# Optimization experiments

Hardware: AMD Instinct MI355X
Metric: run time of the kernel (lower is better)

## Reference

```python
import jax, jax.numpy as jnp
import numpy as np

B, S, E, HID, NTR, NCAL, CW, VOCAB, POS = 4096, 201, 32, 512, 4, 8, 16, 32, 256
LN_EPS = 1e-5


def _ln(x, g, b):
    m = x.mean(-1, keepdims=True)
    v = ((x - m) ** 2).mean(-1, keepdims=True)
    return (x - m) * jax.lax.rsqrt(v + LN_EPS) * g + b


def setup_inputs() -> dict:
    key = jax.random.key(0)
    ks = jax.random.split(key, 24)
    g = lambda i, shape, s=0.1: (jax.random.normal(ks[i], shape, jnp.float32) * s)
    return dict(
        encoded_seq=jax.random.randint(ks[0], (B, S), 0, VOCAB, jnp.int32),
        experiment_id=jax.random.randint(ks[1], (B,), 0, NCAL, jnp.int32),
        tok_emb=g(2, (VOCAB, E), 1.0),
        pos_emb=g(3, (POS, E), 1.0),
        ln1_g=jnp.ones((NTR, E)), ln1_b=jnp.zeros((NTR, E)),
        wq=g(4, (NTR, E, E)), wk=g(5, (NTR, E, E)), wv=g(6, (NTR, E, E)),
        bq=g(7, (NTR, E), 0.01), bk=g(8, (NTR, E), 0.01), bv=g(9, (NTR, E), 0.01),
        wo=g(10, (NTR, E, E)), bo=g(11, (NTR, E), 0.01),
        ln2_g=jnp.ones((NTR, E)), ln2_b=jnp.zeros((NTR, E)),
        w1=g(12, (NTR, E, HID)), b1=g(13, (NTR, HID), 0.01),
        w2=g(14, (NTR, HID, E)), b2=g(15, (NTR, E), 0.01),
        lnf_g=jnp.ones((E,)), lnf_b=jnp.zeros((E,)),
        wpen=g(16, (E, 1)), bpen=g(17, (1,), 0.01),
        wfan=g(18, (1, CW)), bfan=g(19, (CW,), 0.01),
        wcal=g(20, (NCAL, CW, 1)), bcal=g(21, (NCAL, 1), 0.01),
    )


def reference(encoded_seq, experiment_id, tok_emb, pos_emb,
              ln1_g, ln1_b, wq, wk, wv, bq, bk, bv, wo, bo,
              ln2_g, ln2_b, w1, b1, w2, b2,
              lnf_g, lnf_b, wpen, bpen, wfan, bfan, wcal, bcal):
    # embedding + positional add: [B,S,E]
    x = tok_emb[encoded_seq] + pos_emb[jnp.arange(S)]
    scale = 1.0 / jnp.sqrt(jnp.float32(E))  # num_heads=1 => head_dim=E
    for i in range(NTR):
        n = _ln(x, ln1_g[i], ln1_b[i])
        q = n @ wq[i] + bq[i]
        k = n @ wk[i] + bk[i]
        v = n @ wv[i] + bv[i]
        a = jax.nn.softmax(jnp.einsum('bqe,bke->bqk', q, k) * scale, axis=-1)
        att = jnp.einsum('bqk,bke->bqe', a, v) @ wo[i] + bo[i]
        x = x + att
        h = _ln(x, ln2_g[i], ln2_b[i])
        x = x + (jax.nn.silu(h @ w1[i] + b1[i]) @ w2[i] + b2[i])
    contrib = _ln(x, lnf_g, lnf_b) @ wpen + bpen        # [B,S,1]
    underlying = contrib.sum(axis=-2)                    # [B,1]
    pre = jax.nn.elu(underlying @ wfan + bfan)           # [B,CW]
    # all calibrator heads at once: [B,NCAL]
    all_corr = jnp.einsum('bc,ncj->bn', pre, wcal) + bcal[:, 0]
    mask = jax.nn.one_hot(experiment_id, NCAL, dtype=pre.dtype)  # exactly the (exp==id) mask-sum
    corrected = (all_corr * mask).sum(-1, keepdims=True) + underlying
    return corrected.squeeze()
```

## Files before the change

### kernel.cpp

```cpp
#include <hip/hip_runtime.h>


#define SS   201
#define SP   208
#define NMT  13
#define EE   32
#define HIDN 512
#define NTRL 4
#define CWN  16
#define BB   4096
#define XST  36
#define K2ST 20
#define VWST 108

#define X_OFF    0
#define K2_OFF   14976
#define VW2_OFF  31616
#define SMEM_SZ  45440

#define WS_FRAG  0
#define WS_BIAS  294912
#define WS_B1    299008
#define WS_FIN   307200
#define L2E      1.4426950408889634f
#define QCE      0.2550546813f

typedef unsigned short u16;
typedef unsigned int   u32;
typedef short bf16x4 __attribute__((ext_vector_type(4)));
typedef short bf16x8 __attribute__((ext_vector_type(8)));
typedef float f32x4  __attribute__((ext_vector_type(4)));
typedef float f32x2  __attribute__((ext_vector_type(2)));

__device__ __forceinline__ f32x4 MF(bf16x8 a, bf16x8 b, f32x4 c){
  return __builtin_amdgcn_mfma_f32_16x16x32_bf16(a, b, c, 0, 0, 0);
}
__device__ __forceinline__ float bf2f(u16 u){ return __uint_as_float(((u32)u)<<16); }
__device__ __forceinline__ u16 f2bf(float f){
  u32 u = __float_as_uint(f);
  u += 0x7fffu + ((u>>16)&1u);
  return (u16)(u>>16);
}
__device__ __forceinline__ u32 pk2bf(f32x2 v){
#if defined(__has_builtin) && __has_builtin(__builtin_amdgcn_cvt_pk_bf16_f32)
  auto r = __builtin_amdgcn_cvt_pk_bf16_f32(v.x, v.y);
  u32 u; __builtin_memcpy(&u, &r, 4); return u;
#else
  return ((__float_as_uint(v.x)+0x8000u)>>16) | ((__float_as_uint(v.y)+0x8000u) & 0xffff0000u);
#endif
}
__device__ __forceinline__ f32x2 upk2(u32 d){
  return f32x2{ __uint_as_float(d<<16), __uint_as_float(d & 0xffff0000u) };
}
template<bool F32>
__device__ __forceinline__ float ldv(const void* p, int i){
  if (F32) return ((const float*)p)[i];
  return bf2f(((const u16*)p)[i]);
}
template<bool F32>
__device__ __forceinline__ u16 ldbf(const void* p, int i){
  if (F32) return f2bf(((const float*)p)[i]);
  return ((const u16*)p)[i];
}
__device__ __forceinline__ bf16x8 mk8(u32 a0, u32 a1, u32 a2, u32 a3){
  u32 t[4] = {a0,a1,a2,a3};
  bf16x8 r; __builtin_memcpy(&r, t, 16); return r;
}
__device__ __forceinline__ bf16x8 dup8(bf16x4 v){
  bf16x8 r = {v[0],v[0],v[1],v[1],v[2],v[2],v[3],v[3]};
  return r;
}
__device__ __forceinline__ u32 spk(f32x2 z){
  const f32x2 nl2e2 = {-L2E, -L2E};
  const f32x2 one2  = {1.f, 1.f};
  f32x2 a = z * nl2e2;
  f32x2 e = { __builtin_amdgcn_exp2f(a.x), __builtin_amdgcn_exp2f(a.y) };
  f32x2 d = one2 + e;
  f32x2 rc = { __builtin_amdgcn_rcpf(d.x), __builtin_amdgcn_rcpf(d.y) };
  f32x2 s = z * rc;
  return pk2bf(s);
}

__device__ __forceinline__ int sniff_bf16(const void* tok_emb, int tid){
  int sane = 0;
  if (tid < 64){
    u16 wd = ((const u16*)tok_emb)[tid];
    int e = (wd >> 7) & 0xFF;
    sane = (e >= 100 && e <= 140) ? 1 : 0;
  }
  return (__syncthreads_count(sane) >= 52) ? 1 : 0;
}

template<bool F32>
__device__ __forceinline__ void frag_body(const void* wq, const void* wk,
    const void* wv, const void* wo, const void* w1, const void* w2, void* ws)
{
  int t = blockIdx.x;
  int l = t / 72, k = t % 72;
  int lane = threadIdx.x, l16 = lane & 15, quad = lane >> 4;
  bf16x8 v;
  if (k < 8){
    int mat = k >> 1, half = k & 1;
    if (mat == 2){
      int col = half*16 + l16;
      #pragma unroll
      for (int j=0;j<8;j++){
        int a = quad*8 + j;
        float acc = 0.f;
        for (int e=0;e<EE;e++)
          acc += ldv<F32>(wv, l*1024 + a*32 + e) * ldv<F32>(wo, l*1024 + e*32 + col);
        v[j] = (short)f2bf(acc);
      }
    } else if (mat == 0){
      #pragma unroll
      for (int j=0;j<8;j++)
        v[j] = (short)f2bf(QCE * ldv<F32>(wq, l*1024 + (quad*8+j)*32 + half*16 + l16));
    } else {
      const void* src = (mat==1)? wk : wo;
      #pragma unroll
      for (int j=0;j<8;j++)
        v[j] = (short)ldbf<F32>(src, l*1024 + (quad*8+j)*32 + half*16 + l16);
    }
  } else if (k < 40){
    int nt = k - 8;
    #pragma unroll
    for (int j=0;j<8;j++)
      v[j] = (short)ldbf<F32>(w1, l*16384 + (quad*8+j)*512 + nt*16 + l16);
  } else {
    int kc = (k-40)>>1, nh = (k-40)&1;
    #pragma unroll
    for (int j=0;j<8;j++){
      int hh = kc*32 + ((j&4) ? 16 : 0) + quad*4 + (j&3);
      v[j] = (short)ldbf<F32>(w2, l*16384 + hh*32 + nh*16 + l16);
    }
  }
  *(bf16x8*)((char*)ws + WS_FRAG + t*1024 + lane*16) = v;
}

__global__ __launch_bounds__(64) void fmt_frags(
    const void* __restrict__ tok_emb,
    const void* __restrict__ wq, const void* __restrict__ wk,
    const void* __restrict__ wv, const void* __restrict__ wo,
    const void* __restrict__ w1, const void* __restrict__ w2,
    void* __restrict__ ws)
{
  if (sniff_bf16(tok_emb, threadIdx.x)) frag_body<false>(wq,wk,wv,wo,w1,w2,ws);
  else                                  frag_body<true >(wq,wk,wv,wo,w1,w2,ws);
}

template<bool F32>
__device__ __forceinline__ void bias_body(
    const void* bq, const void* bk, const void* bv, const void* wo, const void* bo,
    const void* ln1_g, const void* ln1_b, const void* ln2_g, const void* ln2_b,
    const void* b1, const void* b2,
    const void* lnf_g, const void* lnf_b, const void* wpen, const void* bpen,
    const void* wfan, const void* bfan, const void* wcal, const void* bcal,
    void* ws)
{
  int tid = threadIdx.x, idx = tid & 31, grp = tid >> 5;
  float* BW  = (float*)((char*)ws + WS_BIAS);
  float* BW1 = (float*)((char*)ws + WS_B1);
  float* FW  = (float*)((char*)ws + WS_FIN);
  for (int l=0;l<NTRL;l++){
    float v = 0.f;
    switch(grp){
      case 0: v = QCE * ldv<F32>(bq, l*32+idx); break;
      case 1: v = ldv<F32>(bk, l*32+idx); break;
      case 2: {
        float acc = ldv<F32>(bo, l*32+idx);
        for (int e=0;e<EE;e++) acc += ldv<F32>(bv, l*32+e) * ldv<F32>(wo, l*1024 + e*32 + idx);
        v = acc; break;
      }
      case 3: v = ldv<F32>(ln1_g, l*32+idx); break;
      case 4: v = ldv<F32>(ln1_b, l*32+idx); break;
      case 5: v = ldv<F32>(ln2_g, l*32+idx); break;
      case 6: v = ldv<F32>(ln2_b, l*32+idx); break;
      case 7: v = ldv<F32>(b2,   l*32+idx); break;
    }
    BW[l*256 + tid] = v;
  }
  for (int i=tid; i<NTRL*HIDN; i+=256) BW1[i] = ldv<F32>(b1, i);
  if (tid < 32){
    FW[tid]    = ldv<F32>(lnf_g, tid);
    FW[32+tid] = ldv<F32>(lnf_b, tid);
    FW[64+tid] = ldv<F32>(wpen, tid);
  }
  if (tid == 0) FW[96] = ldv<F32>(bpen, 0);
  if (tid < 16){ FW[97+tid] = ldv<F32>(wfan, tid); FW[113+tid] = ldv<F32>(bfan, tid); }
  if (tid < 128) FW[129+tid] = ldv<F32>(wcal, tid);
  if (tid < 8)   FW[257+tid] = ldv<F32>(bcal, tid);
}

__global__ __launch_bounds__(256) void fmt_bias(
    const void* __restrict__ tok_emb,
    const void* __restrict__ bq, const void* __restrict__ bk,
    const void* __restrict__ bv, const void* __restrict__ wo, const void* __restrict__ bo,
    const void* __restrict__ ln1_g, const void* __restrict__ ln1_b,
    const void* __restrict__ ln2_g, const void* __restrict__ ln2_b,
    const void* __restrict__ b1, const void* __restrict__ b2,
    const void* __restrict__ lnf_g, const void* __restrict__ lnf_b,
    const void* __restrict__ wpen, const void* __restrict__ bpen,
    const void* __restrict__ wfan, const void* __restrict__ bfan,
    const void* __restrict__ wcal, const void* __restrict__ bcal,
    void* __restrict__ ws)
{
  if (sniff_bf16(tok_emb, threadIdx.x))
    bias_body<false>(bq,bk,bv,wo,bo,ln1_g,ln1_b,ln2_g,ln2_b,b1,b2,
                     lnf_g,lnf_b,wpen,bpen,wfan,bfan,wcal,bcal,ws);
  else
    bias_body<true >(bq,bk,bv,wo,bo,ln1_g,ln1_b,ln2_g,ln2_b,b1,b2,
                     lnf_g,lnf_b,wpen,bpen,wfan,bfan,wcal,bcal,ws);
}

__device__ __forceinline__ bf16x8 nfrag_reg(const u16* Xb, int row, int quad,
                                            float m, float rs,
                                            const f32x2* G2, const f32x2* B2){
  const u32* raw = (const u32*)(Xb + row*XST + quad*8);
  f32x2 m2 = {m, m}, rs2 = {rs, rs};
  u32 o[4];
  #pragma unroll
  for (int p=0;p<4;p++){
    f32x2 x = upk2(raw[p]);
    o[p] = pk2bf((x - m2) * rs2 * G2[p] + B2[p]);
  }
  bf16x8 r; __builtin_memcpy(&r, o, 16);
  return r;
}

__device__ __forceinline__ void red_stats(float ps, float pq, float& m, float& rs){
  ps += __shfl_xor(ps, 16); ps += __shfl_xor(ps, 32);
  pq += __shfl_xor(pq, 16); pq += __shfl_xor(pq, 32);
  m  = ps * (1.f/EE);
  rs = rsqrtf(pq * (1.f/EE) - m*m + 1e-5f);
}

template<bool F32>
__device__ __forceinline__ void tr_body(
    const int* seq, const int* expid,
    const void* tok_emb, const void* pos_emb,
    const void* ws, void* out, unsigned char* smem)
{
  u16* Xb  = (u16*)(smem + X_OFF);
  u32* K2  = (u32*)(smem + K2_OFF);
  u16* VW2 = (u16*)(smem + VW2_OFF);
  const int tid  = threadIdx.x;
  const int lane = tid & 63, w = tid >> 6;
  const int l16  = lane & 15, quad = lane >> 4;
  const int b    = blockIdx.x;
  const f32x4 Z  = {0.f,0.f,0.f,0.f};

  {
    const int* srow = seq + b*SS;
    for (int i = tid; i < SP*EE; i += 256){
      int s = i >> 5, e = i & 31;
      float val = 0.f;
      if (s < SS){
        int tok = srow[s];
        val = ldv<F32>(tok_emb, tok*EE + e) + ldv<F32>(pos_emb, s*EE + e);
      }
      Xb[s*XST + e] = f2bf(val);
    }
  }
  __syncthreads();

  float m1[4], rs1[4], m2v[4], rs2v[4];
  #pragma unroll
  for (int t=0;t<4;t++){
    int m = w + 4*t;
    if (m < NMT){
      const u32* raw = (const u32*)(Xb + (m*16+l16)*XST + quad*8);
      f32x2 s2 = {0.f,0.f}, q2 = {0.f,0.f};
      #pragma unroll
      for (int p=0;p<4;p++){ f32x2 x = upk2(raw[p]); s2 += x; q2 += x*x; }
      red_stats(s2.x+s2.y, q2.x+q2.y, m1[t], rs1[t]);
    }
  }

  for (int l = 0; l < NTRL; ++l){
    const char* wsl = (const char*)ws + WS_FRAG + l*73728;
    const float* BW = (const float*)((const char*)ws + WS_BIAS) + l*256;
    bf16x8 bwq0 = *(const bf16x8*)(wsl + 0*1024 + lane*16);
    bf16x8 bwq1 = *(const bf16x8*)(wsl + 1*1024 + lane*16);
    bf16x8 bwk0 = *(const bf16x8*)(wsl + 2*1024 + lane*16);
    bf16x8 bwk1 = *(const bf16x8*)(wsl + 3*1024 + lane*16);
    bf16x8 bwv0 = *(const bf16x8*)(wsl + 4*1024 + lane*16);
    bf16x8 bwv1 = *(const bf16x8*)(wsl + 5*1024 + lane*16);

    bf16x8 aq[4];
    {
      f32x2 G2[4], B2[4];
      #pragma unroll
      for (int p=0;p<4;p++){
        G2[p] = f32x2{BW[96+quad*8+2*p],  BW[96+quad*8+2*p+1]};
        B2[p] = f32x2{BW[128+quad*8+2*p], BW[128+quad*8+2*p+1]};
      }
      f32x4 bq0 = *(const f32x4*)(BW + quad*4);
      f32x4 bq1 = *(const f32x4*)(BW + 16 + quad*4);
      float bk0s = BW[32+l16], bk1s = BW[48+l16];
      f32x4 kc0 = {bk0s,bk0s,bk0s,bk0s};
      f32x4 kc1 = {bk1s,bk1s,bk1s,bk1s};
      #pragma unroll
      for (int t=0;t<4;t++){
        int m = w + 4*t;
        if (m < NMT){
          int m16 = m*16;
          bf16x8 an = nfrag_reg(Xb, m16+l16, quad, m1[t], rs1[t], G2, B2);
          f32x4 ck0 = MF(an, bwk0, kc0), ck1 = MF(an, bwk1, kc1);
          #pragma unroll
          for (int r=0;r<4;r++)
            K2[(m16 + quad*4 + r)*K2ST + l16] = pk2bf(f32x2{ck0[r], ck1[r]});
          f32x4 cw0 = MF(an, bwv0, Z), cw1 = MF(an, bwv1, Z);
          if (m == 12){
            #pragma unroll
            for (int r=0;r<4;r++){
              u32 pk = pk2bf(f32x2{cw0[r], cw1[r]});
              VW2[l16*(2*VWST)      + 192 + quad*4 + r] = (u16)pk;
              VW2[(16+l16)*(2*VWST) + 192 + quad*4 + r] = (u16)(pk>>16);
            }
          } else {
            #pragma unroll
            for (int r=0;r<4;r++){
              u32 pk = pk2bf(f32x2{cw0[r], cw1[r]});
              int colu = ((m>>1)*16 + quad*4 + r)*2 + (m&1);
              VW2[l16*(2*VWST)      + colu] = (u16)pk;
              VW2[(16+l16)*(2*VWST) + colu] = (u16)(pk>>16);
            }
          }
          f32x4 cq0 = MF(bwq0, an, bq0), cq1 = MF(bwq1, an, bq1);
          aq[t] = mk8(pk2bf(f32x2{cq0[0],cq1[0]}), pk2bf(f32x2{cq0[1],cq1[1]}),
                      pk2bf(f32x2{cq0[2],cq1[2]}), pk2bf(f32x2{cq0[3],cq1[3]}));
        }
      }
    }
    __syncthreads();

    {
      const u32* vb0 = (const u32*)VW2 + l16*VWST;
      const u32* vb1 = (const u32*)VW2 + (16+l16)*VWST;
      f32x4 ob0 = *(const f32x4*)(BW + 64 + quad*4);
      f32x4 ob1 = *(const f32x4*)(BW + 80 + quad*4);
      #pragma unroll
      for (int t=0;t<4;t++){
        int m = w + 4*t;
        if (m < NMT){
          int m16 = m*16;
          u32 pbw[7][4];
          f32x2 pacc = {0.f, 0.f};
          #pragma unroll
          for (int c=0;c<6;c++){
            const bf16x8 ka = *(const bf16x8*)(K2 + ((2*c  )*16+l16)*K2ST + quad*4);
            const bf16x8 kb = *(const bf16x8*)(K2 + ((2*c+1)*16+l16)*K2ST + quad*4);
            f32x4 S0 = MF(ka, aq[t], Z);
            f32x4 S1 = MF(kb, aq[t], Z);
            f32x2 ea0 = { __builtin_amdgcn_exp2f(S0[0]), __builtin_amdgcn_exp2f(S0[1]) };
            f32x2 eb0 = { __builtin_amdgcn_exp2f(S0[2]), __builtin_amdgcn_exp2f(S0[3]) };
            f32x2 ea1 = { __builtin_amdgcn_exp2f(S1[0]), __builtin_amdgcn_exp2f(S1[1]) };
            f32x2 eb1 = { __builtin_amdgcn_exp2f(S1[2]), __builtin_amdgcn_exp2f(S1[3]) };
            pacc += (ea0 + eb0) + (ea1 + eb1);
            pbw[c][0] = pk2bf(f32x2{ea0.x, ea1.x});
            pbw[c][1] = pk2bf(f32x2{ea0.y, ea1.y});
            pbw[c][2] = pk2bf(f32x2{eb0.x, eb1.x});
            pbw[c][3] = pk2bf(f32x2{eb0.y, eb1.y});
          }
          {
            const bf16x8 ka = *(const bf16x8*)(K2 + (12*16+l16)*K2ST + quad*4);
            f32x4 S0 = MF(ka, aq[t], Z);
            f32x2 ea0 = { __builtin_amdgcn_exp2f(S0[0]), __builtin_amdgcn_exp2f(S0[1]) };
            f32x2 eb0 = { __builtin_amdgcn_exp2f(S0[2]), __builtin_amdgcn_exp2f(S0[3]) };
            int kb_ = quad*4;
            if (kb_+0 >= 9) ea0.x = 0.f;
            if (kb_+1 >= 9) ea0.y = 0.f;
            if (kb_+2 >= 9) eb0.x = 0.f;
            if (kb_+3 >= 9) eb0.y = 0.f;
            pacc += ea0 + eb0;
            pbw[6][0] = pk2bf(f32x2{ea0.x, 0.f});
            pbw[6][1] = pk2bf(f32x2{ea0.y, 0.f});
            pbw[6][2] = pk2bf(f32x2{eb0.x, 0.f});
            pbw[6][3] = pk2bf(f32x2{eb0.y, 0.f});
          }
          float part = pacc.x + pacc.y;
          part += __shfl_xor(part, 16);
          part += __shfl_xor(part, 32);
          float inv = __builtin_amdgcn_rcpf(part);

          f32x4 o0 = Z, o1 = Z;
          #pragma unroll
          for (int c=0;c<6;c++){
            bf16x8 A0 = *(const bf16x8*)(vb0 + c*16 + quad*4);
            bf16x8 A1 = *(const bf16x8*)(vb1 + c*16 + quad*4);
            bf16x8 B8 = mk8(pbw[c][0], pbw[c][1], pbw[c][2], pbw[c][3]);
            o0 = MF(A0, B8, o0);
            o1 = MF(A1, B8, o1);
          }
          {
            bf16x4 a0l = *(const bf16x4*)((const u16*)vb0 + 192 + quad*4);
            bf16x4 a1l = *(const bf16x4*)((const u16*)vb1 + 192 + quad*4);
            bf16x8 B8 = mk8(pbw[6][0], pbw[6][1], pbw[6][2], pbw[6][3]);
            o0 = MF(dup8(a0l), B8, o0);
            o1 = MF(dup8(a1l), B8, o1);
          }

          u32* xr = (u32*)(Xb + (m16+l16)*XST);
          u32 d0 = xr[quad*2], d1 = xr[quad*2+1];
          f32x2 r01 = f32x2{o0[0],o0[1]} * inv + (upk2(d0) + f32x2{ob0[0],ob0[1]});
          f32x2 r23 = f32x2{o0[2],o0[3]} * inv + (upk2(d1) + f32x2{ob0[2],ob0[3]});
          xr[quad*2]   = pk2bf(r01);
          xr[quad*2+1] = pk2bf(r23);
          u32 d2 = xr[8+quad*2], d3 = xr[8+quad*2+1];
          f32x2 s01 = f32x2{o1[0],o1[1]} * inv + (upk2(d2) + f32x2{ob1[0],ob1[1]});
          f32x2 s23 = f32x2{o1[2],o1[3]} * inv + (upk2(d3) + f32x2{ob1[2],ob1[3]});
          xr[8+quad*2]   = pk2bf(s01);
          xr[8+quad*2+1] = pk2bf(s23);
          f32x2 ss = (r01 + r23) + (s01 + s23);
          f32x2 qq = r01*r01; qq += r23*r23; qq += s01*s01; qq += s23*s23;
          red_stats(ss.x+ss.y, qq.x+qq.y, m2v[t], rs2v[t]);
        }
      }
    }
    __syncthreads();

    {
      f32x2 G2[4], B2[4];
      #pragma unroll
      for (int p=0;p<4;p++){
        G2[p] = f32x2{BW[160+quad*8+2*p], BW[160+quad*8+2*p+1]};
        B2[p] = f32x2{BW[192+quad*8+2*p], BW[192+quad*8+2*p+1]};
      }
      bf16x8 anc[4];
      #pragma unroll
      for (int t=0;t<4;t++){
        int m = w + 4*t;
        if (m < NMT) anc[t] = nfrag_reg(Xb, m*16+l16, quad, m2v[t], rs2v[t], G2, B2);
      }
      f32x4 oacc[4][2];
      #pragma unroll
      for (int t=0;t<4;t++){ oacc[t][0] = Z; oacc[t][1] = Z; }
      const char* w1f = wsl + 8*1024;
      const char* w2f = wsl + 40*1024;
      const float* BW1 = (const float*)((const char*)ws + WS_B1) + l*HIDN;

      for (int hp = 0; hp < 16; ++hp){
        bf16x8 a1lo = *(const bf16x8*)(w1f + (2*hp  )*1024 + lane*16);
        bf16x8 a1hi = *(const bf16x8*)(w1f + (2*hp+1)*1024 + lane*16);
        bf16x8 a2e0 = *(const bf16x8*)(w2f + (hp*2  )*1024 + lane*16);
        bf16x8 a2e1 = *(const bf16x8*)(w2f + (hp*2+1)*1024 + lane*16);
        f32x4 b1q0 = *(const f32x4*)(BW1 + hp*32      + quad*4);
        f32x4 b1q1 = *(const f32x4*)(BW1 + hp*32 + 16 + quad*4);
        #pragma unroll
        for (int t=0;t<4;t++){
          int m = w + 4*t;
          if (m < NMT){
            f32x4 z0 = MF(a1lo, anc[t], b1q0);
            f32x4 z1 = MF(a1hi, anc[t], b1q1);
            bf16x8 H8 = mk8(spk(f32x2{z0[0], z0[1]}), spk(f32x2{z0[2], z0[3]}),
                            spk(f32x2{z1[0], z1[1]}), spk(f32x2{z1[2], z1[3]}));
            oacc[t][0] = MF(a2e0, H8, oacc[t][0]);
            oacc[t][1] = MF(a2e1, H8, oacc[t][1]);
          }
        }
      }

      f32x4 b2q0 = *(const f32x4*)(BW + 224 + quad*4);
      f32x4 b2q1 = *(const f32x4*)(BW + 240 + quad*4);
      #pragma unroll
      for (int t=0;t<4;t++){
        int m = w + 4*t;
        if (m < NMT){
          u32* xr = (u32*)(Xb + (m*16 + l16)*XST);
          u32 d0 = xr[quad*2], d1 = xr[quad*2+1];
          f32x2 r01 = f32x2{oacc[t][0][0], oacc[t][0][1]} + (upk2(d0) + f32x2{b2q0[0], b2q0[1]});
          f32x2 r23 = f32x2{oacc[t][0][2], oacc[t][0][3]} + (upk2(d1) + f32x2{b2q0[2], b2q0[3]});
          xr[quad*2]   = pk2bf(r01);
          xr[quad*2+1] = pk2bf(r23);
          u32 d2 = xr[8+quad*2], d3 = xr[8+quad*2+1];
          f32x2 s01 = f32x2{oacc[t][1][0], oacc[t][1][1]} + (upk2(d2) + f32x2{b2q1[0], b2q1[1]});
          f32x2 s23 = f32x2{oacc[t][1][2], oacc[t][1][3]} + (upk2(d3) + f32x2{b2q1[2], b2q1[3]});
          xr[8+quad*2]   = pk2bf(s01);
          xr[8+quad*2+1] = pk2bf(s23);
          f32x2 ss = (r01 + r23) + (s01 + s23);
          f32x2 qq = r01*r01; qq += r23*r23; qq += s01*s01; qq += s23*s23;
          red_stats(ss.x+ss.y, qq.x+qq.y, m1[t], rs1[t]);
        }
      }
      asm volatile("" ::: "memory");
    }
  }
  __syncthreads();

  const float* FW = (const float*)((const char*)ws + WS_FIN);
  float* HB = (float*)(smem + K2_OFF);
  if (tid < 32){
    HB[tid]    = FW[tid];
    HB[32+tid] = FW[32+tid];
    HB[64+tid] = FW[64+tid];
  }
  __syncthreads();
  float part = 0.f;
  if (tid < SS){
    const u32* row = (const u32*)(Xb + tid*XST);
    f32x2 v[16]; f32x2 s2 = {0.f,0.f};
    #pragma unroll
    for (int i=0;i<16;i++){ f32x2 p = upk2(row[i]); v[i] = p; s2 += p; }
    float m = (s2.x+s2.y) * (1.f/EE);
    f32x2 m2 = {m,m};
    f32x2 var2 = {0.f,0.f};
    #pragma unroll
    for (int i=0;i<16;i++){ f32x2 d = v[i]-m2; var2 += d*d; }
    float rs = rsqrtf((var2.x+var2.y)*(1.f/EE) + 1e-5f);
    f32x2 rs2 = {rs, rs};
    f32x2 dot2 = {0.f,0.f};
    #pragma unroll
    for (int i=0;i<16;i++){
      f32x2 g  = {HB[2*i], HB[2*i+1]};
      f32x2 bb = {HB[32+2*i], HB[33+2*i]};
      f32x2 wp = {HB[64+2*i], HB[65+2*i]};
      dot2 += ((v[i]-m2)*rs2*g + bb) * wp;
    }
    part = dot2.x + dot2.y + FW[96];
  }
  #pragma unroll
  for (int off=32; off; off>>=1) part += __shfl_xor(part, off);
  float* REDF = (float*)(smem + K2_OFF + 1024);
  __syncthreads();
  if (lane == 0) REDF[w] = part;
  __syncthreads();
  if (tid == 0){
    float u = REDF[0] + REDF[1] + REDF[2] + REDF[3];
    int ex = expid[b];
    float corr = FW[257+ex];
    #pragma unroll
    for (int c = 0; c < CWN; ++c){
      float pre = u * FW[97+c] + FW[113+c];
      pre = pre > 0.f ? pre : (__expf(pre) - 1.f);
      corr += pre * FW[129 + ex*CWN + c];
    }
    float res = corr + u;
    if (F32) ((float*)out)[b] = res;
    else     ((u16*)out)[b]  = f2bf(res);
  }
}

__global__ __launch_bounds__(256, 3) void tr_kernel(
    const int* __restrict__ seq, const int* __restrict__ expid,
    const void* __restrict__ tok_emb, const void* __restrict__ pos_emb,
    const void* __restrict__ ws, void* __restrict__ out)
{
  __shared__ __align__(16) unsigned char smem[SMEM_SZ];
  if (sniff_bf16(tok_emb, threadIdx.x))
    tr_body<false>(seq, expid, tok_emb, pos_emb, ws, out, smem);
  else
    tr_body<true >(seq, expid, tok_emb, pos_emb, ws, out, smem);
}

extern "C" void kernel_launch(void* const* d_in, const int* in_sizes, int n_in,
                              void* d_out, int out_size, void* d_ws, size_t ws_size,
                              hipStream_t stream)
{
  (void)in_sizes; (void)n_in; (void)ws_size; (void)out_size;
  const void* tok_emb = d_in[2];
  fmt_frags<<<dim3(288), dim3(64), 0, stream>>>(
      tok_emb, d_in[6], d_in[7], d_in[8], d_in[12], d_in[16], d_in[18], d_ws);
  fmt_bias<<<dim3(1), dim3(256), 0, stream>>>(
      tok_emb, d_in[9], d_in[10], d_in[11], d_in[12], d_in[13],
      d_in[4], d_in[5], d_in[14], d_in[15], d_in[17], d_in[19],
      d_in[20], d_in[21], d_in[22], d_in[23],
      d_in[24], d_in[25], d_in[26], d_in[27], d_ws);
  tr_kernel<<<dim3(BB), dim3(256), 0, stream>>>(
      (const int*)d_in[0], (const int*)d_in[1], tok_emb, d_in[3], d_ws, d_out);
}
```

Baseline: 884.2 us.

## Keep residual stream in registers and permute weight fragment row order

The per-token residual activations now stay in registers (xp) in MFMA fragment layout for all layers, replacing the shared-memory X buffer and its loads and stores. Weight fragments are pre-permuted so that LayerNorm output, attention probabilities and VW2 stores line up with register ownership, which allows packed 32-bit stores and simpler P packing. Shared memory shrinks, which may allow more blocks per CU, but register pressure rises and the final LN stage needs one extra smem spill.

```diff
diff --git a/kernel.cpp b/kernel.cpp
--- a/kernel.cpp
+++ b/kernel.cpp
@@ -9,14 +9,11 @@
 #define NTRL 4
 #define CWN  16
 #define BB   4096
-#define XST  36
 #define K2ST 20
-#define VWST 108
-
-#define X_OFF    0
-#define K2_OFF   14976
-#define VW2_OFF  31616
-#define SMEM_SZ  45440
+#define VWST 216
+
+#define VW2_OFF  16640
+#define SMEM_SZ  30464
 
 #define WS_FRAG  0
 #define WS_BIAS  294912
@@ -62,13 +59,13 @@
   if (F32) return f2bf(((const float*)p)[i]);
   return ((const u16*)p)[i];
 }
+__device__ __forceinline__ bf16x8 cat44(bf16x4 lo, bf16x4 hi){
+  bf16x8 r = {lo[0],lo[1],lo[2],lo[3],hi[0],hi[1],hi[2],hi[3]};
+  return r;
+}
 __device__ __forceinline__ bf16x8 mk8(u32 a0, u32 a1, u32 a2, u32 a3){
   u32 t[4] = {a0,a1,a2,a3};
   bf16x8 r; __builtin_memcpy(&r, t, 16); return r;
-}
-__device__ __forceinline__ bf16x8 dup8(bf16x4 v){
-  bf16x8 r = {v[0],v[0],v[1],v[1],v[2],v[2],v[3],v[3]};
-  return r;
 }
 __device__ __forceinline__ u32 spk(f32x2 z){
   const f32x2 nl2e2 = {-L2E, -L2E};
@@ -105,27 +102,33 @@
       int col = half*16 + l16;
       #pragma unroll
       for (int j=0;j<8;j++){
-        int a = quad*8 + j;
+        int pr = quad*4 + (j&3) + ((j&4)<<2);
         float acc = 0.f;
         for (int e=0;e<EE;e++)
-          acc += ldv<F32>(wv, l*1024 + a*32 + e) * ldv<F32>(wo, l*1024 + e*32 + col);
+          acc += ldv<F32>(wv, l*1024 + pr*32 + e) * ldv<F32>(wo, l*1024 + e*32 + col);
         v[j] = (short)f2bf(acc);
       }
     } else if (mat == 0){
       #pragma unroll
-      for (int j=0;j<8;j++)
-        v[j] = (short)f2bf(QCE * ldv<F32>(wq, l*1024 + (quad*8+j)*32 + half*16 + l16));
+      for (int j=0;j<8;j++){
+        int pr = quad*4 + (j&3) + ((j&4)<<2);
+        v[j] = (short)f2bf(QCE * ldv<F32>(wq, l*1024 + pr*32 + half*16 + l16));
+      }
     } else {
       const void* src = (mat==1)? wk : wo;
       #pragma unroll
-      for (int j=0;j<8;j++)
-        v[j] = (short)ldbf<F32>(src, l*1024 + (quad*8+j)*32 + half*16 + l16);
+      for (int j=0;j<8;j++){
+        int pr = quad*4 + (j&3) + ((j&4)<<2);
+        v[j] = (short)ldbf<F32>(src, l*1024 + pr*32 + half*16 + l16);
+      }
     }
   } else if (k < 40){
     int nt = k - 8;
     #pragma unroll
-    for (int j=0;j<8;j++)
-      v[j] = (short)ldbf<F32>(w1, l*16384 + (quad*8+j)*512 + nt*16 + l16);
+    for (int j=0;j<8;j++){
+      int pr = quad*4 + (j&3) + ((j&4)<<2);
+      v[j] = (short)ldbf<F32>(w1, l*16384 + pr*512 + nt*16 + l16);
+    }
   } else {
     int kc = (k-40)>>1, nh = (k-40)&1;
     #pragma unroll
@@ -212,17 +215,14 @@
                      lnf_g,lnf_b,wpen,bpen,wfan,bfan,wcal,bcal,ws);
 }
 
-__device__ __forceinline__ bf16x8 nfrag_reg(const u16* Xb, int row, int quad,
-                                            float m, float rs,
-                                            const f32x2* G2, const f32x2* B2){
-  const u32* raw = (const u32*)(Xb + row*XST + quad*8);
+__device__ __forceinline__ bf16x8 nfrag_x(const u32* xp, float m, float rs,
+                                          f32x4 ga, f32x4 gb, f32x4 ba, f32x4 bb){
   f32x2 m2 = {m, m}, rs2 = {rs, rs};
   u32 o[4];
-  #pragma unroll
-  for (int p=0;p<4;p++){
-    f32x2 x = upk2(raw[p]);
-    o[p] = pk2bf((x - m2) * rs2 * G2[p] + B2[p]);
-  }
+  o[0] = pk2bf((upk2(xp[0]) - m2) * rs2 * f32x2{ga[0],ga[1]} + f32x2{ba[0],ba[1]});
+  o[1] = pk2bf((upk2(xp[1]) - m2) * rs2 * f32x2{ga[2],ga[3]} + f32x2{ba[2],ba[3]});
+  o[2] = pk2bf((upk2(xp[2]) - m2) * rs2 * f32x2{gb[0],gb[1]} + f32x2{bb[0],bb[1]});
+  o[3] = pk2bf((upk2(xp[3]) - m2) * rs2 * f32x2{gb[2],gb[3]} + f32x2{bb[2],bb[3]});
   bf16x8 r; __builtin_memcpy(&r, o, 16);
   return r;
 }
@@ -240,39 +240,41 @@
     const void* tok_emb, const void* pos_emb,
     const void* ws, void* out, unsigned char* smem)
 {
-  u16* Xb  = (u16*)(smem + X_OFF);
-  u32* K2  = (u32*)(smem + K2_OFF);
+  u32* K2  = (u32*)smem;
   u16* VW2 = (u16*)(smem + VW2_OFF);
+
   const int tid  = threadIdx.x;
   const int lane = tid & 63, w = tid >> 6;
   const int l16  = lane & 15, quad = lane >> 4;
   const int b    = blockIdx.x;
   const f32x4 Z  = {0.f,0.f,0.f,0.f};
 
+  u32 xp[4][4];
+  float m1[4], rs1[4], m2v[4], rs2v[4];
   {
     const int* srow = seq + b*SS;
-    for (int i = tid; i < SP*EE; i += 256){
-      int s = i >> 5, e = i & 31;
-      float val = 0.f;
-      if (s < SS){
-        int tok = srow[s];
-        val = ldv<F32>(tok_emb, tok*EE + e) + ldv<F32>(pos_emb, s*EE + e);
-      }
-      Xb[s*XST + e] = f2bf(val);
-    }
-  }
-  __syncthreads();
-
-  float m1[4], rs1[4], m2v[4], rs2v[4];
-  #pragma unroll
-  for (int t=0;t<4;t++){
-    int m = w + 4*t;
-    if (m < NMT){
-      const u32* raw = (const u32*)(Xb + (m*16+l16)*XST + quad*8);
-      f32x2 s2 = {0.f,0.f}, q2 = {0.f,0.f};
-      #pragma unroll
-      for (int p=0;p<4;p++){ f32x2 x = upk2(raw[p]); s2 += x; q2 += x*x; }
-      red_stats(s2.x+s2.y, q2.x+q2.y, m1[t], rs1[t]);
+    #pragma unroll
+    for (int t=0;t<4;t++){
+      int m = w + 4*t;
+      if (m < NMT){
+        int row = m*16 + l16;
+        if (row < SS){
+          int tok = srow[row];
+          #pragma unroll
+          for (int p=0;p<4;p++){
+            int c = (p<2) ? (quad*4 + 2*p) : (16 + quad*4 + 2*(p-2));
+            f32x2 v = { ldv<F32>(tok_emb, tok*EE + c)   + ldv<F32>(pos_emb, row*EE + c),
+                        ldv<F32>(tok_emb, tok*EE + c+1) + ldv<F32>(pos_emb, row*EE + c+1) };
+            xp[t][p] = pk2bf(v);
+          }
+        } else {
+          xp[t][0]=0u; xp[t][1]=0u; xp[t][2]=0u; xp[t][3]=0u;
+        }
+        f32x2 s2 = {0.f,0.f}, q2 = {0.f,0.f};
+        #pragma unroll
+        for (int p=0;p<4;p++){ f32x2 x = upk2(xp[t][p]); s2 += x; q2 += x*x; }
+        red_stats(s2.x+s2.y, q2.x+q2.y, m1[t], rs1[t]);
+      }
     }
   }
 
@@ -288,12 +290,10 @@
 
     bf16x8 aq[4];
     {
-      f32x2 G2[4], B2[4];
-      #pragma unroll
-      for (int p=0;p<4;p++){
-        G2[p] = f32x2{BW[96+quad*8+2*p],  BW[96+quad*8+2*p+1]};
-        B2[p] = f32x2{BW[128+quad*8+2*p], BW[128+quad*8+2*p+1]};
-      }
+      f32x4 ga = *(const f32x4*)(BW + 96 + quad*4);
+      f32x4 gb = *(const f32x4*)(BW + 112 + quad*4);
+      f32x4 ba = *(const f32x4*)(BW + 128 + quad*4);
+      f32x4 bb = *(const f32x4*)(BW + 144 + quad*4);
       f32x4 bq0 = *(const f32x4*)(BW + quad*4);
       f32x4 bq1 = *(const f32x4*)(BW + 16 + quad*4);
       float bk0s = BW[32+l16], bk1s = BW[48+l16];
@@ -304,27 +304,21 @@
         int m = w + 4*t;
         if (m < NMT){
           int m16 = m*16;
-          bf16x8 an = nfrag_reg(Xb, m16+l16, quad, m1[t], rs1[t], G2, B2);
+          bf16x8 an = nfrag_x(xp[t], m1[t], rs1[t], ga, gb, ba, bb);
           f32x4 ck0 = MF(an, bwk0, kc0), ck1 = MF(an, bwk1, kc1);
           #pragma unroll
           for (int r=0;r<4;r++)
             K2[(m16 + quad*4 + r)*K2ST + l16] = pk2bf(f32x2{ck0[r], ck1[r]});
           f32x4 cw0 = MF(an, bwv0, Z), cw1 = MF(an, bwv1, Z);
-          if (m == 12){
-            #pragma unroll
-            for (int r=0;r<4;r++){
-              u32 pk = pk2bf(f32x2{cw0[r], cw1[r]});
-              VW2[l16*(2*VWST)      + 192 + quad*4 + r] = (u16)pk;
-              VW2[(16+l16)*(2*VWST) + 192 + quad*4 + r] = (u16)(pk>>16);
-            }
-          } else {
-            #pragma unroll
-            for (int r=0;r<4;r++){
-              u32 pk = pk2bf(f32x2{cw0[r], cw1[r]});
-              int colu = ((m>>1)*16 + quad*4 + r)*2 + (m&1);
-              VW2[l16*(2*VWST)      + colu] = (u16)pk;
-              VW2[(16+l16)*(2*VWST) + colu] = (u16)(pk>>16);
-            }
+          {
+            int base = (m == 12) ? (192 + quad*4)
+                                 : ((m>>1)*32 + quad*8 + (m&1)*4);
+            u32* p0 = (u32*)(VW2 + l16*VWST + base);
+            u32* p1 = (u32*)(VW2 + (16+l16)*VWST + base);
+            p0[0] = pk2bf(f32x2{cw0[0], cw0[1]});
+            p0[1] = pk2bf(f32x2{cw0[2], cw0[3]});
+            p1[0] = pk2bf(f32x2{cw1[0], cw1[1]});
+            p1[1] = pk2bf(f32x2{cw1[2], cw1[3]});
           }
           f32x4 cq0 = MF(bwq0, an, bq0), cq1 = MF(bwq1, an, bq1);
           aq[t] = mk8(pk2bf(f32x2{cq0[0],cq1[0]}), pk2bf(f32x2{cq0[1],cq1[1]}),
@@ -335,15 +329,14 @@
     __syncthreads();
 
     {
-      const u32* vb0 = (const u32*)VW2 + l16*VWST;
-      const u32* vb1 = (const u32*)VW2 + (16+l16)*VWST;
+      const u16* vb0 = VW2 + l16*VWST;
+      const u16* vb1 = VW2 + (16+l16)*VWST;
       f32x4 ob0 = *(const f32x4*)(BW + 64 + quad*4);
       f32x4 ob1 = *(const f32x4*)(BW + 80 + quad*4);
       #pragma unroll
       for (int t=0;t<4;t++){
         int m = w + 4*t;
         if (m < NMT){
-          int m16 = m*16;
           u32 pbw[7][4];
           f32x2 pacc = {0.f, 0.f};
           #pragma unroll
@@ -357,10 +350,10 @@
             f32x2 ea1 = { __builtin_amdgcn_exp2f(S1[0]), __builtin_amdgcn_exp2f(S1[1]) };
             f32x2 eb1 = { __builtin_amdgcn_exp2f(S1[2]), __builtin_amdgcn_exp2f(S1[3]) };
             pacc += (ea0 + eb0) + (ea1 + eb1);
-            pbw[c][0] = pk2bf(f32x2{ea0.x, ea1.x});
-            pbw[c][1] = pk2bf(f32x2{ea0.y, ea1.y});
-            pbw[c][2] = pk2bf(f32x2{eb0.x, eb1.x});
-            pbw[c][3] = pk2bf(f32x2{eb0.y, eb1.y});
+            pbw[c][0] = pk2bf(ea0);
+            pbw[c][1] = pk2bf(eb0);
+            pbw[c][2] = pk2bf(ea1);
+            pbw[c][3] = pk2bf(eb1);
           }
           {
             const bf16x8 ka = *(const bf16x8*)(K2 + (12*16+l16)*K2ST + quad*4);
@@ -373,10 +366,10 @@
             if (kb_+2 >= 9) eb0.x = 0.f;
             if (kb_+3 >= 9) eb0.y = 0.f;
             pacc += ea0 + eb0;
-            pbw[6][0] = pk2bf(f32x2{ea0.x, 0.f});
-            pbw[6][1] = pk2bf(f32x2{ea0.y, 0.f});
-            pbw[6][2] = pk2bf(f32x2{eb0.x, 0.f});
-            pbw[6][3] = pk2bf(f32x2{eb0.y, 0.f});
+            pbw[6][0] = pk2bf(ea0);
+            pbw[6][1] = pk2bf(eb0);
+            pbw[6][2] = 0u;
+            pbw[6][3] = 0u;
           }
           float part = pacc.x + pacc.y;
           part += __shfl_xor(part, 16);
@@ -386,31 +379,28 @@
           f32x4 o0 = Z, o1 = Z;
           #pragma unroll
           for (int c=0;c<6;c++){
-            bf16x8 A0 = *(const bf16x8*)(vb0 + c*16 + quad*4);
-            bf16x8 A1 = *(const bf16x8*)(vb1 + c*16 + quad*4);
+            bf16x8 A0 = *(const bf16x8*)(vb0 + c*32 + quad*8);
+            bf16x8 A1 = *(const bf16x8*)(vb1 + c*32 + quad*8);
             bf16x8 B8 = mk8(pbw[c][0], pbw[c][1], pbw[c][2], pbw[c][3]);
             o0 = MF(A0, B8, o0);
             o1 = MF(A1, B8, o1);
           }
           {
-            bf16x4 a0l = *(const bf16x4*)((const u16*)vb0 + 192 + quad*4);
-            bf16x4 a1l = *(const bf16x4*)((const u16*)vb1 + 192 + quad*4);
-            bf16x8 B8 = mk8(pbw[6][0], pbw[6][1], pbw[6][2], pbw[6][3]);
-            o0 = MF(dup8(a0l), B8, o0);
-            o1 = MF(dup8(a1l), B8, o1);
-          }
-
-          u32* xr = (u32*)(Xb + (m16+l16)*XST);
-          u32 d0 = xr[quad*2], d1 = xr[quad*2+1];
-          f32x2 r01 = f32x2{o0[0],o0[1]} * inv + (upk2(d0) + f32x2{ob0[0],ob0[1]});
-          f32x2 r23 = f32x2{o0[2],o0[3]} * inv + (upk2(d1) + f32x2{ob0[2],ob0[3]});
-          xr[quad*2]   = pk2bf(r01);
-          xr[quad*2+1] = pk2bf(r23);
-          u32 d2 = xr[8+quad*2], d3 = xr[8+quad*2+1];
-          f32x2 s01 = f32x2{o1[0],o1[1]} * inv + (upk2(d2) + f32x2{ob1[0],ob1[1]});
-          f32x2 s23 = f32x2{o1[2],o1[3]} * inv + (upk2(d3) + f32x2{ob1[2],ob1[3]});
-          xr[8+quad*2]   = pk2bf(s01);
-          xr[8+quad*2+1] = pk2bf(s23);
+            bf16x4 a0 = *(const bf16x4*)(vb0 + 192 + quad*4);
+            bf16x4 a1 = *(const bf16x4*)(vb1 + 192 + quad*4);
+            bf16x8 B8 = mk8(pbw[6][0], pbw[6][1], 0u, 0u);
+            o0 = MF(cat44(a0, a0), B8, o0);
+            o1 = MF(cat44(a1, a1), B8, o1);
+          }
+
+          f32x2 r01 = f32x2{o0[0],o0[1]} * inv + (upk2(xp[t][0]) + f32x2{ob0[0],ob0[1]});
+          f32x2 r23 = f32x2{o0[2],o0[3]} * inv + (upk2(xp[t][1]) + f32x2{ob0[2],ob0[3]});
+          f32x2 s01 = f32x2{o1[0],o1[1]} * inv + (upk2(xp[t][2]) + f32x2{ob1[0],ob1[1]});
+          f32x2 s23 = f32x2{o1[2],o1[3]} * inv + (upk2(xp[t][3]) + f32x2{ob1[2],ob1[3]});
+          xp[t][0] = pk2bf(r01);
+          xp[t][1] = pk2bf(r23);
+          xp[t][2] = pk2bf(s01);
+          xp[t][3] = pk2bf(s23);
           f32x2 ss = (r01 + r23) + (s01 + s23);
           f32x2 qq = r01*r01; qq += r23*r23; qq += s01*s01; qq += s23*s23;
           red_stats(ss.x+ss.y, qq.x+qq.y, m2v[t], rs2v[t]);
@@ -420,17 +410,15 @@
     __syncthreads();
 
     {
-      f32x2 G2[4], B2[4];
-      #pragma unroll
-      for (int p=0;p<4;p++){
-        G2[p] = f32x2{BW[160+quad*8+2*p], BW[160+quad*8+2*p+1]};
-        B2[p] = f32x2{BW[192+quad*8+2*p], BW[192+quad*8+2*p+1]};
-      }
+      f32x4 ga = *(const f32x4*)(BW + 160 + quad*4);
+      f32x4 gb = *(const f32x4*)(BW + 176 + quad*4);
+      f32x4 ba = *(const f32x4*)(BW + 192 + quad*4);
+      f32x4 bb = *(const f32x4*)(BW + 208 + quad*4);
       bf16x8 anc[4];
       #pragma unroll
       for (int t=0;t<4;t++){
         int m = w + 4*t;
-        if (m < NMT) anc[t] = nfrag_reg(Xb, m*16+l16, quad, m2v[t], rs2v[t], G2, B2);
+        if (m < NMT) anc[t] = nfrag_x(xp[t], m2v[t], rs2v[t], ga, gb, ba, bb);
       }
       f32x4 oacc[4][2];
       #pragma unroll
@@ -466,38 +454,45 @@
       for (int t=0;t<4;t++){
         int m = w + 4*t;
         if (m < NMT){
-          u32* xr = (u32*)(Xb + (m*16 + l16)*XST);
-          u32 d0 = xr[quad*2], d1 = xr[quad*2+1];
-          f32x2 r01 = f32x2{oacc[t][0][0], oacc[t][0][1]} + (upk2(d0) + f32x2{b2q0[0], b2q0[1]});
-          f32x2 r23 = f32x2{oacc[t][0][2], oacc[t][0][3]} + (upk2(d1) + f32x2{b2q0[2], b2q0[3]});
-          xr[quad*2]   = pk2bf(r01);
-          xr[quad*2+1] = pk2bf(r23);
-          u32 d2 = xr[8+quad*2], d3 = xr[8+quad*2+1];
-          f32x2 s01 = f32x2{oacc[t][1][0], oacc[t][1][1]} + (upk2(d2) + f32x2{b2q1[0], b2q1[1]});
-          f32x2 s23 = f32x2{oacc[t][1][2], oacc[t][1][3]} + (upk2(d3) + f32x2{b2q1[2], b2q1[3]});
-          xr[8+quad*2]   = pk2bf(s01);
-          xr[8+quad*2+1] = pk2bf(s23);
+          f32x2 r01 = f32x2{oacc[t][0][0], oacc[t][0][1]} + (upk2(xp[t][0]) + f32x2{b2q0[0], b2q0[1]});
+          f32x2 r23 = f32x2{oacc[t][0][2], oacc[t][0][3]} + (upk2(xp[t][1]) + f32x2{b2q0[2], b2q0[3]});
+          f32x2 s01 = f32x2{oacc[t][1][0], oacc[t][1][1]} + (upk2(xp[t][2]) + f32x2{b2q1[0], b2q1[1]});
+          f32x2 s23 = f32x2{oacc[t][1][2], oacc[t][1][3]} + (upk2(xp[t][3]) + f32x2{b2q1[2], b2q1[3]});
+          xp[t][0] = pk2bf(r01);
+          xp[t][1] = pk2bf(r23);
+          xp[t][2] = pk2bf(s01);
+          xp[t][3] = pk2bf(s23);
           f32x2 ss = (r01 + r23) + (s01 + s23);
           f32x2 qq = r01*r01; qq += r23*r23; qq += s01*s01; qq += s23*s23;
           red_stats(ss.x+ss.y, qq.x+qq.y, m1[t], rs1[t]);
         }
       }
-      asm volatile("" ::: "memory");
-    }
-  }
-  __syncthreads();
+    }
+  }
 
   const float* FW = (const float*)((const char*)ws + WS_FIN);
-  float* HB = (float*)(smem + K2_OFF);
+  float* HB = (float*)(smem + VW2_OFF);
   if (tid < 32){
     HB[tid]    = FW[tid];
     HB[32+tid] = FW[32+tid];
     HB[64+tid] = FW[64+tid];
   }
+  u32* hd = (u32*)smem;
+  #pragma unroll
+  for (int t=0;t<4;t++){
+    int m = w + 4*t;
+    if (m < NMT){
+      u32* hr = hd + (m*16 + l16)*18;
+      hr[quad*2]     = xp[t][0];
+      hr[quad*2+1]   = xp[t][1];
+      hr[8+quad*2]   = xp[t][2];
+      hr[8+quad*2+1] = xp[t][3];
+    }
+  }
   __syncthreads();
   float part = 0.f;
   if (tid < SS){
-    const u32* row = (const u32*)(Xb + tid*XST);
+    const u32* row = hd + tid*18;
     f32x2 v[16]; f32x2 s2 = {0.f,0.f};
     #pragma unroll
     for (int i=0;i<16;i++){ f32x2 p = upk2(row[i]); v[i] = p; s2 += p; }
@@ -520,7 +515,7 @@
   }
   #pragma unroll
   for (int off=32; off; off>>=1) part += __shfl_xor(part, off);
-  float* REDF = (float*)(smem + K2_OFF + 1024);
+  float* REDF = (float*)(smem + VW2_OFF + 512);
   __syncthreads();
   if (lane == 0) REDF[w] = part;
   __syncthreads();
```

After: 916.9 us. +3.7%, slower.
